# Optimization experiments

Hardware: AMD Instinct MI355X
Metric: run time of the kernel (lower is better)

Reference implementation:

```python
import jax, jax.numpy as jnp
import numpy as np

N0, N1, N2 = 200_000, 100_000, 80_000
F = 32
K5, K3 = 125, 27
M1, M2, M3, M4 = 20_000, 20_000, 30_000, 20_000
EPS = 1e-5


def sparse_conv(feats, W, in_idx, out_idx, n_out):
    """Gather-GEMM-scatter sparse conv. feats:[Nin,Cin], W:[K,Cin,Cout],
    in_idx/out_idx:[K,M] kernel map. Returns [n_out, Cout]."""
    g = feats[in_idx]                                  # [K, M, Cin] gather
    contrib = jnp.einsum('kmc,kcd->kmd', g, W)         # per-offset GEMM
    cout = W.shape[-1]
    out = jnp.zeros((n_out, cout), feats.dtype)
    return out.at[out_idx.reshape(-1)].add(contrib.reshape(-1, cout))


def bn(x, g, b):
    m = x.mean(0)
    v = x.var(0)
    return (x - m) * jax.lax.rsqrt(v + EPS) * g + b


def setup_inputs():
    key = jax.random.key(0)
    ks = jax.random.split(key, 16)
    W_SCALE = 0.02
    inp = {
        'x_feats': jax.random.normal(ks[0], (N0, 1), jnp.float32),
        'w1a': jax.random.normal(ks[1], (K5, 1, F), jnp.float32) * W_SCALE,
        'w1b': jax.random.normal(ks[2], (K5, F, F), jnp.float32) * W_SCALE,
        'w1c': jax.random.normal(ks[3], (K5, F, F), jnp.float32) * W_SCALE,
        'w2': jax.random.normal(ks[4], (K3, F, 2 * F), jnp.float32) * W_SCALE,
        'w3a': jax.random.normal(ks[5], (K3, 2 * F, 4 * F), jnp.float32) * W_SCALE,
        'w3b': jax.random.normal(ks[6], (K3, 4 * F, 8 * F), jnp.float32) * W_SCALE,
        'bn1b_g': jnp.ones((F,), jnp.float32), 'bn1b_b': jnp.zeros((F,), jnp.float32),
        'bn1c_g': jnp.ones((F,), jnp.float32), 'bn1c_b': jnp.zeros((F,), jnp.float32),
        'bn3a_g': jnp.ones((4 * F,), jnp.float32), 'bn3a_b': jnp.zeros((4 * F,), jnp.float32),
        'bn3b_g': jnp.ones((8 * F,), jnp.float32), 'bn3b_b': jnp.zeros((8 * F,), jnp.float32),
        'km1a_in': jax.random.randint(ks[7], (K5, M1), 0, N0, jnp.int32),
        'km1a_out': jax.random.randint(ks[8], (K5, M1), 0, N1, jnp.int32),
        'km1b_in': jax.random.randint(ks[9], (K5, M2), 0, N1, jnp.int32),
        'km1b_out': jax.random.randint(ks[10], (K5, M2), 0, N1, jnp.int32),
        'km1c_in': jax.random.randint(ks[11], (K5, M2), 0, N1, jnp.int32),
        'km1c_out': jax.random.randint(ks[12], (K5, M2), 0, N1, jnp.int32),
        'km2_in': jax.random.randint(ks[13], (K3, M3), 0, N1, jnp.int32),
        'km2_out': jax.random.randint(ks[14], (K3, M3), 0, N2, jnp.int32),
        'km3a_in': jax.random.randint(jax.random.fold_in(key, 20), (K3, M4), 0, N2, jnp.int32),
        'km3a_out': jax.random.randint(jax.random.fold_in(key, 21), (K3, M4), 0, N2, jnp.int32),
        'km3b_in': jax.random.randint(jax.random.fold_in(key, 22), (K3, M4), 0, N2, jnp.int32),
        'km3b_out': jax.random.randint(jax.random.fold_in(key, 23), (K3, M4), 0, N2, jnp.int32),
        'n1': N1,
        'n2': N2,
    }
    return inp


def reference(x_feats, w1a, w1b, w1c, w2, w3a, w3b,
              bn1b_g, bn1b_b, bn1c_g, bn1c_b, bn3a_g, bn3a_b, bn3b_g, bn3b_b,
              km1a_in, km1a_out, km1b_in, km1b_out, km1c_in, km1c_out,
              km2_in, km2_out, km3a_in, km3a_out, km3b_in, km3b_out, n1, n2):
    # enc1: conv(1->F, k5, s2) + ReLU
    h = jax.nn.relu(sparse_conv(x_feats, w1a, km1a_in, km1a_out, n1))
    # conv(F->F, k5) + BN + ReLU
    h = jax.nn.relu(bn(sparse_conv(h, w1b, km1b_in, km1b_out, n1), bn1b_g, bn1b_b))
    # conv(F->F, k5) + BN + ReLU
    x_e1 = jax.nn.relu(bn(sparse_conv(h, w1c, km1c_in, km1c_out, n1), bn1c_g, bn1c_b))
    # conv2: conv(F->2F, k3) onto c_out coordinates (no activation)
    h2 = sparse_conv(x_e1, w2, km2_in, km2_out, n2)
    # enc2: conv(2F->4F, k3) + BN + ReLU
    h2 = jax.nn.relu(bn(sparse_conv(h2, w3a, km3a_in, km3a_out, n2), bn3a_g, bn3a_b))
    # conv(4F->8F, k3) + BN + ReLU
    x_e2 = jax.nn.relu(bn(sparse_conv(h2, w3b, km3b_in, km3b_out, n2), bn3b_g, bn3b_b))
    return (x_e1, x_e2)
```

## Files before the change

kernel.cpp:

```cpp
#include <hip/hip_runtime.h>
#include <hip/hip_fp16.h>
#include <cstdint>
#include <algorithm>

#define N1c 100000
#define N2c 80000
#define EPSc 1e-5f
#define STRIDE_N1 102400
#define STRIDE_N2 81920

__global__ __launch_bounds__(256) void rank2d_kernel(
    const int* __restrict__ out_idx, int* __restrict__ rank,
    int* __restrict__ bins, int E, int M, int q, int stride)
{
    for (int e = blockIdx.x * 256 + threadIdx.x; e < E; e += gridDim.x * 256) {
        int chunk = (e / M) / q;
        rank[e] = atomicAdd(&bins[chunk * stride + out_idx[e]], 1);
    }
}

__global__ __launch_bounds__(256) void scan1(
    const int* __restrict__ bins, int* __restrict__ ptr,
    int* __restrict__ bsums, int n)
{
    __shared__ int lds[256];
    int base = blockIdx.x * 1024;
    int v[4]; int t = 0;
    #pragma unroll
    for (int i = 0; i < 4; ++i) {
        int idx = base + threadIdx.x * 4 + i;
        v[i] = idx < n ? bins[idx] : 0;
        t += v[i];
    }
    lds[threadIdx.x] = t; __syncthreads();
    for (int off = 1; off < 256; off <<= 1) {
        int x = threadIdx.x >= off ? lds[threadIdx.x - off] : 0;
        __syncthreads();
        lds[threadIdx.x] += x;
        __syncthreads();
    }
    int run = lds[threadIdx.x] - t;
    if (threadIdx.x == 255) bsums[blockIdx.x] = lds[255];
    #pragma unroll
    for (int i = 0; i < 4; ++i) {
        int idx = base + threadIdx.x * 4 + i;
        if (idx < n) ptr[idx] = run;
        run += v[i];
    }
}

__global__ __launch_bounds__(64) void scan2s(
    int* __restrict__ bsums, int bpc, int nch)
{
    int c = threadIdx.x;
    if (c < nch) {
        int run = 0;
        for (int i = 0; i < bpc; ++i) {
            int idx = c * bpc + i;
            int t = bsums[idx]; bsums[idx] = run; run += t;
        }
    }
}

__global__ __launch_bounds__(256) void scan3(
    int* __restrict__ ptr, const int* __restrict__ bsums, int n)
{
    int idx = blockIdx.x * 1024 + threadIdx.x * 4;
    int add = bsums[blockIdx.x];
    #pragma unroll
    for (int i = 0; i < 4; ++i)
        if (idx + i < n) ptr[idx + i] += add;
}

__global__ __launch_bounds__(256) void scatter_1a(
    const float* __restrict__ x, const int* __restrict__ iin,
    const int* __restrict__ iout, const int* __restrict__ ptr,
    const int* __restrict__ rank, float2* __restrict__ payload, int E, int M)
{
    for (int e = blockIdx.x * 256 + threadIdx.x; e < E; e += gridDim.x * 256) {
        int k = e / M;
        float2 p; p.x = x[iin[e]]; p.y = __int_as_float(k);
        payload[ptr[iout[e]] + rank[e]] = p;
    }
}

__global__ __launch_bounds__(256) void phaseB_1a(
    const float2* __restrict__ payload, const int* __restrict__ ptr,
    const float* __restrict__ W, float* __restrict__ out, int n)
{
    __shared__ float Wl[125 * 32];
    for (int i = threadIdx.x; i < 125 * 32; i += 256) Wl[i] = W[i];
    __syncthreads();
    int total = n * 32;
    for (int idx = blockIdx.x * 256 + threadIdx.x; idx < total; idx += gridDim.x * 256) {
        int o = idx >> 5, c = idx & 31;
        int s0 = ptr[o], s1 = ptr[o + 1];
        float acc = 0.f;
        for (int s = s0; s < s1; ++s) {
            float2 p = payload[s];
            acc = fmaf(p.x, Wl[(__float_as_int(p.y) << 5) + c], acc);
        }
        out[idx] = fmaxf(acc, 0.f);
    }
}

template <int CIN, int CINC, int CTILE, int WST, int TP, int TC, int GMODE>
__global__ __launch_bounds__(256) void phaseA8(
    const float* __restrict__ feats, const float* __restrict__ W,
    const int* __restrict__ in_idx, const int* __restrict__ out_idx,
    const int* __restrict__ ptr, const int* __restrict__ rank,
    __half* __restrict__ contrib, int M,
    const float* __restrict__ sc, const float* __restrict__ sh)
{
    constexpr int NCG = CTILE / TC;
    constexpr int PPG = 256 / NCG;
    constexpr int PP  = PPG * TP;
    constexpr int NCH  = CIN / CINC;
    constexpr int LOADERS = 256 / PP;
    constexpr int SITER = CINC / 4 / LOADERS;
    constexpr int FTS = PP + 4;
    static_assert(SITER >= 1, "CINC too small for loader layout");

    const int k = blockIdx.y;
    __shared__ float Wl[CINC][CTILE];
    __shared__ float ft[CINC][FTS];
    __shared__ int sslot[PP];

    const int cg = threadIdx.x % NCG;
    const int pg = threadIdx.x / NCG;
    const int p0 = pg * TP;
    const int pl = threadIdx.x % PP;
    const int ll = threadIdx.x / PP;

    const int* iin  = in_idx  + (size_t)k * M;
    const int* iout = out_idx + (size_t)k * M;
    const int* rk   = rank    + (size_t)k * M;
    const float* Wk = W + (size_t)k * CIN * WST;

    for (int base = blockIdx.x * PP; base < M; base += gridDim.x * PP) {
        float acc[TP][TC];
        #pragma unroll
        for (int p = 0; p < TP; ++p)
            #pragma unroll
            for (int c = 0; c < TC; ++c) acc[p][c] = 0.f;

        int p = base + pl;
        bool act = p < M;
        const float* fr = nullptr;
        float4 v[SITER];
        if (act) {
            fr = feats + (size_t)iin[p] * CIN;
            #pragma unroll
            for (int i = 0; i < SITER; ++i)
                v[i] = *(const float4*)(fr + (ll + i * LOADERS) * 4);
        }

        #pragma unroll
        for (int ch = 0; ch < NCH; ++ch) {
            __syncthreads();
            for (int i = threadIdx.x; i < CINC * (CTILE / 4); i += 256) {
                int j = i / (CTILE / 4), q = i % (CTILE / 4);
                int gq = q % (TC / 4);
                int cq = q / (TC / 4);
                int pq = gq * NCG + cq;
                *(float4*)&Wl[j][pq * 4] =
                    *(const float4*)(Wk + (size_t)(ch * CINC + j) * WST + q * 4);
            }
            if (act) {
                if (ch == 0 && threadIdx.x < PP)
                    sslot[pl] = ptr[iout[p]] + rk[p];
                #pragma unroll
                for (int i = 0; i < SITER; ++i) {
                    int j4 = (ll + i * LOADERS) * 4;
                    float4 w = v[i];
                    if (GMODE == 2) {
                        float4 s4 = *(const float4*)(sc + ch * CINC + j4);
                        float4 h4 = *(const float4*)(sh + ch * CINC + j4);
                        w.x = fmaxf(fmaf(w.x, s4.x, h4.x), 0.f);
                        w.y = fmaxf(fmaf(w.y, s4.y, h4.y), 0.f);
                        w.z = fmaxf(fmaf(w.z, s4.z, h4.z), 0.f);
                        w.w = fmaxf(fmaf(w.w, s4.w, h4.w), 0.f);
                    }
                    ft[j4 + 0][pl] = w.x;
                    ft[j4 + 1][pl] = w.y;
                    ft[j4 + 2][pl] = w.z;
                    ft[j4 + 3][pl] = w.w;
                }
                if (ch + 1 < NCH) {
                    #pragma unroll
                    for (int i = 0; i < SITER; ++i)
                        v[i] = *(const float4*)(fr + (ch + 1) * CINC
                                                + (ll + i * LOADERS) * 4);
                }
            }
            __syncthreads();

            #pragma unroll 4
            for (int j = 0; j < CINC; ++j) {
                float fv[TP], wv[TC];
                #pragma unroll
                for (int g = 0; g < TP / 4; ++g)
                    *(float4*)&fv[g * 4] = *(const float4*)&ft[j][p0 + g * 4];
                #pragma unroll
                for (int g = 0; g < TC / 4; ++g)
                    *(float4*)&wv[g * 4] = *(const float4*)&Wl[j][(g * NCG + cg) * 4];
                #pragma unroll
                for (int pp = 0; pp < TP; ++pp)
                    #pragma unroll
                    for (int c = 0; c < TC; ++c)
                        acc[pp][c] = fmaf(fv[pp], wv[c], acc[pp][c]);
            }
        }

        #pragma unroll
        for (int q = 0; q < TP; ++q) {
            if (base + p0 + q < M) {
                size_t s = (size_t)sslot[p0 + q];
                #pragma unroll
                for (int g = 0; g < TC / 4; ++g) {
                    __half2 h0 = __floats2half2_rn(acc[q][g * 4 + 0], acc[q][g * 4 + 1]);
                    __half2 h1 = __floats2half2_rn(acc[q][g * 4 + 2], acc[q][g * 4 + 3]);
                    uint2 pk;
                    pk.x = *(unsigned int*)&h0;
                    pk.y = *(unsigned int*)&h1;
                    *(uint2*)&contrib[s * CTILE + cg * TC + g * 4] = pk;
                }
            }
        }
    }
}

template <int CSTR, bool STATS>
__global__ __launch_bounds__(256) void phaseB8(
    const __half* __restrict__ contrib, const int* __restrict__ ptr,
    float* __restrict__ out, int n, int ostr, int accum,
    double* __restrict__ statsbuf, int sqoff)
{
    float s1 = 0.f, s2 = 0.f;
    int total = n * CSTR;
    for (int idx = blockIdx.x * 256 + threadIdx.x; idx < total; idx += gridDim.x * 256) {
        int o = idx / CSTR, c = idx % CSTR;
        int a = ptr[o], b = ptr[o + 1];
        float acc = accum ? out[(size_t)o * ostr + c] : 0.f;
        for (int s = a; s < b; ++s)
            acc += __half2float(contrib[(size_t)s * CSTR + c]);
        out[(size_t)o * ostr + c] = acc;
        if (STATS) { s1 += acc; s2 += acc * acc; }
    }
    if constexpr (STATS) {
        __shared__ double l1[256], l2[256];
        l1[threadIdx.x] = (double)s1; l2[threadIdx.x] = (double)s2;
        __syncthreads();
        for (int off = 128; off >= CSTR; off >>= 1) {
            if (threadIdx.x < (unsigned)off) {
                l1[threadIdx.x] += l1[threadIdx.x + off];
                l2[threadIdx.x] += l2[threadIdx.x + off];
            }
            __syncthreads();
        }
        if (threadIdx.x < CSTR) {
            atomicAdd(&statsbuf[threadIdx.x], l1[threadIdx.x]);
            atomicAdd(&statsbuf[sqoff + threadIdx.x], l2[threadIdx.x]);
        }
    }
}

template <int C>
__global__ __launch_bounds__(256) void make_scsh(
    const double* __restrict__ sums, const float* __restrict__ g,
    const float* __restrict__ b, float* __restrict__ sc, float* __restrict__ sh,
    double inv_n)
{
    int c = threadIdx.x;
    if (c < C) {
        double mean = sums[c] * inv_n;
        double var  = sums[C + c] * inv_n - mean * mean;
        float s = g[c] * (float)(1.0 / sqrt(var + (double)EPSc));
        sc[c] = s;
        sh[c] = b[c] - (float)mean * s;
    }
}

template <int C>
__global__ __launch_bounds__(256) void bn_apply_relu_kernel(
    float* __restrict__ x, int n, const double* __restrict__ sums,
    const float* __restrict__ g, const float* __restrict__ b)
{
    const int c = threadIdx.x % C;
    const double inv_n = 1.0 / (double)n;
    double mean = sums[c] * inv_n;
    double var  = sums[C + c] * inv_n - mean * mean;
    float scale = g[c] * (float)(1.0 / sqrt(var + (double)EPSc));
    float shift = b[c] - (float)mean * scale;
    size_t total = (size_t)n * C;
    size_t stride = (size_t)gridDim.x * 256;
    for (size_t i = (size_t)blockIdx.x * 256 + threadIdx.x; i < total; i += stride)
        x[i] = fmaxf(x[i] * scale + shift, 0.f);
}

struct Plan { int q, nch; };

static Plan make_plan(long long tot_elems, int K, long long cap, int maxch)
{
    if (cap < 1) cap = 1;
    long long nch0 = (tot_elems + cap - 1) / cap;
    if (nch0 < 1) nch0 = 1;
    if (nch0 > K) nch0 = K;
    int q = (int)((K + nch0 - 1) / nch0);
    int nch = (K + q - 1) / q;
    if (nch > maxch) { q = (K + maxch - 1) / maxch; nch = (K + q - 1) / q; }
    return { q, nch };
}

static void build_csr2d(const int* iout, int* rank, int* bins, int* ptr, int* bsums,
                        int E, int M, int q, int nch, int stride, hipStream_t s)
{
    hipMemsetAsync(bins, 0, (size_t)nch * stride * sizeof(int), s);
    int gb = std::min(2048, (E + 255) / 256);
    hipLaunchKernelGGL(rank2d_kernel, dim3(gb), dim3(256), 0, s, iout, rank, bins, E, M, q, stride);
    int totalbins = nch * stride, nb = totalbins / 1024, bpc = stride / 1024;
    hipLaunchKernelGGL(scan1, dim3(nb), dim3(256), 0, s, bins, ptr, bsums, totalbins);
    hipLaunchKernelGGL(scan2s, dim3(1), dim3(64), 0, s, bsums, bpc, nch);
    hipLaunchKernelGGL(scan3, dim3(nb), dim3(256), 0, s, ptr, bsums, totalbins);
}

template <int CIN, int CINC, int COUT, int TP, int TC, int GMODE, bool STATS>
static void run_layer(const float* feats, const float* W,
                      const int* iin, const int* iout, float* outp,
                      int M, int K, int n_out, int stride, int maxch,
                      int* bins, int* ptr, int* bsums, int* rank, __half* contrib,
                      long long cap_f32, const float* sc, const float* sh,
                      double* statsbuf, hipStream_t s)
{
    constexpr int NCG = COUT / TC;
    constexpr int PP  = (256 / NCG) * TP;
    long long cap_h = cap_f32 * 2;
    Plan pl = make_plan((long long)K * M * COUT, K, cap_h, maxch);
    build_csr2d(iout, rank, bins, ptr, bsums, K * M, M, pl.q, pl.nch, stride, s);
    for (int ch = 0; ch < pl.nch; ++ch) {
        int k0 = ch * pl.q;
        int qc = std::min(pl.q, K - k0);
        dim3 g((M + PP - 1) / PP, qc);
        hipLaunchKernelGGL((phaseA8<CIN, CINC, COUT, COUT, TP, TC, GMODE>), g, dim3(256), 0, s,
                           feats, W + (size_t)k0 * CIN * COUT,
                           iin + (size_t)k0 * M, iout + (size_t)k0 * M,
                           ptr + (size_t)ch * stride, rank + (size_t)k0 * M,
                           contrib, M, sc, sh);
        bool last = (ch == pl.nch - 1);
        if (STATS && last)
            hipLaunchKernelGGL((phaseB8<COUT, true>), dim3(2048), dim3(256), 0, s,
                               contrib, ptr + (size_t)ch * stride, outp, n_out, COUT,
                               ch ? 1 : 0, statsbuf, COUT);
        else
            hipLaunchKernelGGL((phaseB8<COUT, false>), dim3(2048), dim3(256), 0, s,
                               contrib, ptr + (size_t)ch * stride, outp, n_out, COUT,
                               ch ? 1 : 0, (double*)nullptr, 0);
    }
}

extern "C" void kernel_launch(void* const* d_in, const int* in_sizes, int n_in,
                              void* d_out, int out_size, void* d_ws, size_t ws_size,
                              hipStream_t stream)
{
    const float* x_feats = (const float*)d_in[0];
    const float* w1a = (const float*)d_in[1];
    const float* w1b = (const float*)d_in[2];
    const float* w1c = (const float*)d_in[3];
    const float* w2  = (const float*)d_in[4];
    const float* w3a = (const float*)d_in[5];
    const float* w3b = (const float*)d_in[6];
    const float* bn1b_g = (const float*)d_in[7];
    const float* bn1b_b = (const float*)d_in[8];
    const float* bn1c_g = (const float*)d_in[9];
    const float* bn1c_b = (const float*)d_in[10];
    const float* bn3a_g = (const float*)d_in[11];
    const float* bn3a_b = (const float*)d_in[12];
    const float* bn3b_g = (const float*)d_in[13];
    const float* bn3b_b = (const float*)d_in[14];
    const int* km1a_in  = (const int*)d_in[15];
    const int* km1a_out = (const int*)d_in[16];
    const int* km1b_in  = (const int*)d_in[17];
    const int* km1b_out = (const int*)d_in[18];
    const int* km1c_in  = (const int*)d_in[19];
    const int* km1c_out = (const int*)d_in[20];
    const int* km2_in   = (const int*)d_in[21];
    const int* km2_out  = (const int*)d_in[22];
    const int* km3a_in  = (const int*)d_in[23];
    const int* km3a_out = (const int*)d_in[24];
    const int* km3b_in  = (const int*)d_in[25];
    const int* km3b_out = (const int*)d_in[26];

    float* out  = (float*)d_out;
    float* x_e1 = out;
    float* x_e2 = out + (size_t)N1c * 32;

    float* ws = (float*)d_ws;
    float*  poolA  = ws;
    float*  poolB  = poolA + 10240000;
    double* dstats = (double*)(poolB + 5120000);
    float*  scsh   = (float*)(dstats + 2048);
    int*    bins   = (int*)(scsh + 1024);
    int*    ptr    = bins + 819200;
    int*    bsums  = ptr + 819200;
    int*    rank   = bsums + 1024;
    float*  contribf = (float*)(rank + 2500000);
    __half* contrib  = (__half*)contribf;
    const long long FIXED = 10240000LL + 5120000 + 4096 + 1024
                          + 819200 + 819200 + 1024 + 2500000;
    long long cap = (long long)(ws_size / 4) - FIXED - 32;
    if (cap < 1) cap = 1;

    float* h1  = poolA;
    float* h3  = poolA;
    float* h2  = poolB;
    float* h2b = poolB;

    double* dst1b = dstats;
    double* dst1c = dstats + 512;
    double* dst3a = dstats + 1024;
    double* dst3b = dstats + 1536;
    float* sc1b = scsh,       *sh1b = scsh + 32;
    float* sc3a = scsh + 256, *sh3a = scsh + 384;

    hipMemsetAsync(dstats, 0, 2048 * sizeof(double), stream);

    {
        build_csr2d(km1a_out, rank, bins, ptr, bsums, 125 * 20000, 20000, 125, 1,
                    STRIDE_N1, stream);
        hipLaunchKernelGGL(scatter_1a, dim3(2048), dim3(256), 0, stream,
                           x_feats, km1a_in, km1a_out, ptr, rank, (float2*)contribf,
                           125 * 20000, 20000);
        hipLaunchKernelGGL(phaseB_1a, dim3(2048), dim3(256), 0, stream,
                           (const float2*)contribf, ptr, w1a, h1, N1c);
    }

    run_layer<32, 32, 32, 8, 4, 0, true>(h1, w1b, km1b_in, km1b_out, h2, 20000, 125, N1c,
                                         STRIDE_N1, 8, bins, ptr, bsums, rank, contrib,
                                         cap, nullptr, nullptr, dst1b, stream);
    hipLaunchKernelGGL((make_scsh<32>), dim3(1), dim3(256), 0, stream,
                       dst1b, bn1b_g, bn1b_b, sc1b, sh1b, 1.0 / N1c);

    run_layer<32, 32, 32, 8, 4, 2, true>(h2, w1c, km1c_in, km1c_out, x_e1, 20000, 125, N1c,
                                         STRIDE_N1, 8, bins, ptr, bsums, rank, contrib,
                                         cap, sc1b, sh1b, dst1c, stream);
    hipLaunchKernelGGL((bn_apply_relu_kernel<32>), dim3(2048), dim3(256), 0, stream,
                       x_e1, N1c, dst1c, bn1c_g, bn1c_b);

    run_layer<32, 32, 64, 8, 8, 0, false>(x_e1, w2, km2_in, km2_out, h2b, 30000, 27, N2c,
                                          STRIDE_N2, 10, bins, ptr, bsums, rank, contrib,
                                          cap, nullptr, nullptr, nullptr, stream);

    run_layer<64, 32, 128, 8, 8, 0, true>(h2b, w3a, km3a_in, km3a_out, h3, 20000, 27, N2c,
                                          STRIDE_N2, 10, bins, ptr, bsums, rank, contrib,
                                          cap, nullptr, nullptr, dst3a, stream);
    hipLaunchKernelGGL((make_scsh<128>), dim3(1), dim3(256), 0, stream,
                       dst3a, bn3a_g, bn3a_b, sc3a, sh3a, 1.0 / N2c);

    {
        const int M = 20000, K = 27;
        Plan pl = make_plan((long long)K * M * 128, K, cap * 2, 10);
        build_csr2d(km3b_out, rank, bins, ptr, bsums, K * M, M, pl.q, pl.nch,
                    STRIDE_N2, stream);
        constexpr int PP = (256 / (128 / 8)) * 8;
        for (int half = 0; half < 2; ++half) {
            for (int ch = 0; ch < pl.nch; ++ch) {
                int k0 = ch * pl.q;
                int qc = std::min(pl.q, K - k0);
                dim3 g((M + PP - 1) / PP, qc);
                hipLaunchKernelGGL((phaseA8<128, 32, 128, 256, 8, 8, 2>), g, dim3(256), 0, stream,
                                   h3, w3b + half * 128 + (size_t)k0 * 128 * 256,
                                   km3b_in + (size_t)k0 * M, km3b_out + (size_t)k0 * M,
                                   ptr + (size_t)ch * STRIDE_N2, rank + (size_t)k0 * M,
                                   contrib, M, sc3a, sh3a);
                bool last = (ch == pl.nch - 1);
                if (last)
                    hipLaunchKernelGGL((phaseB8<128, true>), dim3(2048), dim3(256), 0, stream,
                                       contrib, ptr + (size_t)ch * STRIDE_N2,
                                       x_e2 + half * 128, N2c, 256, ch ? 1 : 0,
                                       dst3b + half * 128, 256);
                else
                    hipLaunchKernelGGL((phaseB8<128, false>), dim3(2048), dim3(256), 0, stream,
                                       contrib, ptr + (size_t)ch * STRIDE_N2,
                                       x_e2 + half * 128, N2c, 256, ch ? 1 : 0,
                                       (double*)nullptr, 0);
            }
        }
        hipLaunchKernelGGL((bn_apply_relu_kernel<256>), dim3(2048), dim3(256), 0, stream,
                           x_e2, N2c, dst3b, bn3b_g, bn3b_b);
    }
}
```

Measured before the change: 2.201 ms.

## Use packed fp16 dot2 for gather-GEMM inner product in phaseA8

Converts both the weight tile and the gathered feature tile to packed half2 in shared memory and replaces the fp32 FMA inner loop with v_dot2_f32_f16, which processes two input channels per instruction while accumulating in fp32. This halves LDS footprint and LDS read traffic per multiply and roughly halves ALU instruction count in the GEMM loop. It also drops the register prefetch of the next channel chunk, loading features inside each chunk instead. Inputs are rounded to fp16, which lowers precision.

Result: faster. 2.064 ms (-6.2%).

```diff
diff --git a/kernel.cpp b/kernel.cpp
--- a/kernel.cpp
+++ b/kernel.cpp
@@ -8,6 +8,18 @@
 #define EPSc 1e-5f
 #define STRIDE_N1 102400
 #define STRIDE_N2 81920
+
+typedef _Float16 half2_t __attribute__((ext_vector_type(2)));
+
+__device__ __forceinline__ float dot2(half2_t a, half2_t b, float c)
+{
+#if __has_builtin(__builtin_amdgcn_fdot2)
+    return __builtin_amdgcn_fdot2(a, b, c, false);
+#else
+    asm("v_dot2_f32_f16 %0, %1, %2, %0" : "+v"(c) : "v"(a), "v"(b));
+    return c;
+#endif
+}
 
 __global__ __launch_bounds__(256) void rank2d_kernel(
     const int* __restrict__ out_idx, int* __restrict__ rank,
@@ -120,10 +132,11 @@
     constexpr int SITER = CINC / 4 / LOADERS;
     constexpr int FTS = PP + 4;
     static_assert(SITER >= 1, "CINC too small for loader layout");
+    static_assert((CINC % 2) == 0 && (TP % 4) == 0 && (TC % 4) == 0, "");
 
     const int k = blockIdx.y;
-    __shared__ float Wl[CINC][CTILE];
-    __shared__ float ft[CINC][FTS];
+    __shared__ half2_t Wl[CINC / 2][CTILE];
+    __shared__ half2_t ft[CINC / 2][FTS];
     __shared__ int sslot[PP];
 
     const int cg = threadIdx.x % NCG;
@@ -144,71 +157,64 @@
             #pragma unroll
             for (int c = 0; c < TC; ++c) acc[p][c] = 0.f;
 
-        int p = base + pl;
-        bool act = p < M;
-        const float* fr = nullptr;
-        float4 v[SITER];
-        if (act) {
-            fr = feats + (size_t)iin[p] * CIN;
-            #pragma unroll
-            for (int i = 0; i < SITER; ++i)
-                v[i] = *(const float4*)(fr + (ll + i * LOADERS) * 4);
-        }
-
         #pragma unroll
         for (int ch = 0; ch < NCH; ++ch) {
             __syncthreads();
-            for (int i = threadIdx.x; i < CINC * (CTILE / 4); i += 256) {
-                int j = i / (CTILE / 4), q = i % (CTILE / 4);
+            for (int i = threadIdx.x; i < (CINC / 2) * (CTILE / 4); i += 256) {
+                int j2 = i / (CTILE / 4), q = i % (CTILE / 4);
                 int gq = q % (TC / 4);
                 int cq = q / (TC / 4);
                 int pq = gq * NCG + cq;
-                *(float4*)&Wl[j][pq * 4] =
-                    *(const float4*)(Wk + (size_t)(ch * CINC + j) * WST + q * 4);
-            }
-            if (act) {
+                const float* wr = Wk + (size_t)(ch * CINC + 2 * j2) * WST + q * 4;
+                float4 a = *(const float4*)wr;
+                float4 b = *(const float4*)(wr + WST);
+                half2_t t[4];
+                t[0][0] = (_Float16)a.x; t[0][1] = (_Float16)b.x;
+                t[1][0] = (_Float16)a.y; t[1][1] = (_Float16)b.y;
+                t[2][0] = (_Float16)a.z; t[2][1] = (_Float16)b.z;
+                t[3][0] = (_Float16)a.w; t[3][1] = (_Float16)b.w;
+                *(uint4*)&Wl[j2][pq * 4] = *(uint4*)t;
+            }
+            int p = base + pl;
+            if (p < M) {
                 if (ch == 0 && threadIdx.x < PP)
                     sslot[pl] = ptr[iout[p]] + rk[p];
+                const float* fr = feats + (size_t)iin[p] * CIN + ch * CINC;
                 #pragma unroll
                 for (int i = 0; i < SITER; ++i) {
                     int j4 = (ll + i * LOADERS) * 4;
-                    float4 w = v[i];
+                    float4 v = *(const float4*)(fr + j4);
                     if (GMODE == 2) {
                         float4 s4 = *(const float4*)(sc + ch * CINC + j4);
                         float4 h4 = *(const float4*)(sh + ch * CINC + j4);
-                        w.x = fmaxf(fmaf(w.x, s4.x, h4.x), 0.f);
-                        w.y = fmaxf(fmaf(w.y, s4.y, h4.y), 0.f);
-                        w.z = fmaxf(fmaf(w.z, s4.z, h4.z), 0.f);
-                        w.w = fmaxf(fmaf(w.w, s4.w, h4.w), 0.f);
+                        v.x = fmaxf(fmaf(v.x, s4.x, h4.x), 0.f);
+                        v.y = fmaxf(fmaf(v.y, s4.y, h4.y), 0.f);
+                        v.z = fmaxf(fmaf(v.z, s4.z, h4.z), 0.f);
+                        v.w = fmaxf(fmaf(v.w, s4.w, h4.w), 0.f);
                     }
-                    ft[j4 + 0][pl] = w.x;
-                    ft[j4 + 1][pl] = w.y;
-                    ft[j4 + 2][pl] = w.z;
-                    ft[j4 + 3][pl] = w.w;
+                    half2_t lo, hi;
+                    lo[0] = (_Float16)v.x; lo[1] = (_Float16)v.y;
+                    hi[0] = (_Float16)v.z; hi[1] = (_Float16)v.w;
+                    ft[j4 / 2 + 0][pl] = lo;
+                    ft[j4 / 2 + 1][pl] = hi;
                 }
-                if (ch + 1 < NCH) {
-                    #pragma unroll
-                    for (int i = 0; i < SITER; ++i)
-                        v[i] = *(const float4*)(fr + (ch + 1) * CINC
-                                                + (ll + i * LOADERS) * 4);
-                }
             }
             __syncthreads();
 
             #pragma unroll 4
-            for (int j = 0; j < CINC; ++j) {
-                float fv[TP], wv[TC];
+            for (int j2 = 0; j2 < CINC / 2; ++j2) {
+                half2_t fv[TP], wv[TC];
                 #pragma unroll
                 for (int g = 0; g < TP / 4; ++g)
-                    *(float4*)&fv[g * 4] = *(const float4*)&ft[j][p0 + g * 4];
+                    *(uint4*)&fv[g * 4] = *(const uint4*)&ft[j2][p0 + g * 4];
                 #pragma unroll
                 for (int g = 0; g < TC / 4; ++g)
-                    *(float4*)&wv[g * 4] = *(const float4*)&Wl[j][(g * NCG + cg) * 4];
+                    *(uint4*)&wv[g * 4] = *(const uint4*)&Wl[j2][(g * NCG + cg) * 4];
                 #pragma unroll
                 for (int pp = 0; pp < TP; ++pp)
                     #pragma unroll
                     for (int c = 0; c < TC; ++c)
-                        acc[pp][c] = fmaf(fv[pp], wv[c], acc[pp][c]);
+                        acc[pp][c] = dot2(fv[pp], wv[c], acc[pp][c]);
             }
         }
 
```

## Replace FP32 register-tiled gather-GEMM with fp16 MFMA kernel using swizzled LDS

Applied to the files above, without the earlier changes.

The per-offset gather-GEMM kernel (phaseA8) is rewritten to use the 16x16x32 fp16 MFMA instructions. Gathered features and weights are converted to fp16 and staged in XOR-swizzled shared memory, and each wave computes a 32-row by CTILE-column output tile. This targets the cost of scalar FP32 FMAs in the gather-GEMM stages of all layers. In exchange, inputs are rounded to fp16 before the multiply, and the contrib writes become scalar half stores instead of packed stores, which may add write traffic overhead.

Measured after the change: 1.989 ms. -9.6%, faster.

```diff
diff --git a/kernel.cpp b/kernel.cpp
--- a/kernel.cpp
+++ b/kernel.cpp
@@ -8,6 +8,9 @@
 #define EPSc 1e-5f
 #define STRIDE_N1 102400
 #define STRIDE_N2 81920
+
+typedef _Float16 fp16x8 __attribute__((ext_vector_type(8)));
+typedef float f32x4 __attribute__((ext_vector_type(4)));
 
 __global__ __launch_bounds__(256) void rank2d_kernel(
     const int* __restrict__ out_idx, int* __restrict__ rank,
@@ -104,33 +107,30 @@
     }
 }
 
-template <int CIN, int CINC, int CTILE, int WST, int TP, int TC, int GMODE>
-__global__ __launch_bounds__(256) void phaseA8(
+template <int CIN, int CTILE, int WST, int GMODE>
+__global__ __launch_bounds__(256) void phaseA_mfma(
     const float* __restrict__ feats, const float* __restrict__ W,
     const int* __restrict__ in_idx, const int* __restrict__ out_idx,
     const int* __restrict__ ptr, const int* __restrict__ rank,
     __half* __restrict__ contrib, int M,
     const float* __restrict__ sc, const float* __restrict__ sh)
 {
-    constexpr int NCG = CTILE / TC;
-    constexpr int PPG = 256 / NCG;
-    constexpr int PP  = PPG * TP;
-    constexpr int NCH  = CIN / CINC;
-    constexpr int LOADERS = 256 / PP;
-    constexpr int SITER = CINC / 4 / LOADERS;
-    constexpr int FTS = PP + 4;
-    static_assert(SITER >= 1, "CINC too small for loader layout");
-
-    const int k = blockIdx.y;
-    __shared__ float Wl[CINC][CTILE];
-    __shared__ float ft[CINC][FTS];
+    constexpr int PP  = 128;
+    constexpr int NK  = CIN / 32;
+    constexpr int NCF = CTILE / 16;
+    constexpr int NRF = 2;
+    constexpr int GCHK = (CIN * 2) / 16;
+    constexpr int GSM  = (GCHK < 8 ? GCHK : 8) - 1;
+    static_assert(CIN % 32 == 0 && CTILE % 16 == 0, "");
+
+    __shared__ __align__(16) _Float16 Gl[PP * CIN];
+    __shared__ __align__(16) _Float16 Wt[CTILE * CIN];
     __shared__ int sslot[PP];
 
-    const int cg = threadIdx.x % NCG;
-    const int pg = threadIdx.x / NCG;
-    const int p0 = pg * TP;
-    const int pl = threadIdx.x % PP;
-    const int ll = threadIdx.x / PP;
+    const int tid  = threadIdx.x;
+    const int wave = tid >> 6;
+    const int lane = tid & 63;
+    const int k    = blockIdx.y;
 
     const int* iin  = in_idx  + (size_t)k * M;
     const int* iout = out_idx + (size_t)k * M;
@@ -138,95 +138,109 @@
     const float* Wk = W + (size_t)k * CIN * WST;
 
     for (int base = blockIdx.x * PP; base < M; base += gridDim.x * PP) {
-        float acc[TP][TC];
+        if (tid < PP && base + tid < M)
+            sslot[tid] = ptr[iout[base + tid]] + rk[base + tid];
+
+        {
+            int r  = tid & (PP - 1);
+            int hh = tid >> 7;
+            int p  = base + r;
+            if (p < M) {
+                const int c0 = hh * (CIN / 2);
+                const float* fr = feats + (size_t)iin[p] * CIN + c0;
+                #pragma unroll
+                for (int c = 0; c < CIN / 2; c += 8) {
+                    float a[8];
+                    *(float4*)&a[0] = *(const float4*)(fr + c);
+                    *(float4*)&a[4] = *(const float4*)(fr + c + 4);
+                    if (GMODE == 2) {
+                        float s[8], h[8];
+                        *(float4*)&s[0] = *(const float4*)(sc + c0 + c);
+                        *(float4*)&s[4] = *(const float4*)(sc + c0 + c + 4);
+                        *(float4*)&h[0] = *(const float4*)(sh + c0 + c);
+                        *(float4*)&h[4] = *(const float4*)(sh + c0 + c + 4);
+                        #pragma unroll
+                        for (int j = 0; j < 8; ++j)
+                            a[j] = fmaxf(fmaf(a[j], s[j], h[j]), 0.f);
+                    }
+                    _Float16 t[8];
+                    #pragma unroll
+                    for (int j = 0; j < 8; ++j) t[j] = (_Float16)a[j];
+                    int col = c0 + c;
+                    int idx = r * CIN + ((((col >> 3) ^ (r & GSM))) << 3);
+                    *(uint4*)&Gl[idx] = *(uint4*)t;
+                }
+            }
+        }
+
+        for (int i = tid; i < (CTILE / 4) * (CIN / 4); i += 256) {
+            int c4 = (i % (CTILE / 4)) * 4;
+            int k4 = (i / (CTILE / 4)) * 4;
+            const float* wr = Wk + (size_t)k4 * WST + c4;
+            float a0[4], a1[4], a2[4], a3[4];
+            *(float4*)a0 = *(const float4*)wr;
+            *(float4*)a1 = *(const float4*)(wr + WST);
+            *(float4*)a2 = *(const float4*)(wr + 2 * (size_t)WST);
+            *(float4*)a3 = *(const float4*)(wr + 3 * (size_t)WST);
+            #pragma unroll
+            for (int j = 0; j < 4; ++j) {
+                _Float16 t[4] = { (_Float16)a0[j], (_Float16)a1[j],
+                                  (_Float16)a2[j], (_Float16)a3[j] };
+                int row = c4 + j;
+                int idx = row * CIN + (((k4 >> 3) ^ (row & GSM)) << 3) + (k4 & 7);
+                *(uint2*)&Wt[idx] = *(uint2*)t;
+            }
+        }
+        __syncthreads();
+
+        f32x4 acc[NRF][NCF];
         #pragma unroll
-        for (int p = 0; p < TP; ++p)
+        for (int rf = 0; rf < NRF; ++rf)
             #pragma unroll
-            for (int c = 0; c < TC; ++c) acc[p][c] = 0.f;
-
-        int p = base + pl;
-        bool act = p < M;
-        const float* fr = nullptr;
-        float4 v[SITER];
-        if (act) {
-            fr = feats + (size_t)iin[p] * CIN;
+            for (int cf = 0; cf < NCF; ++cf)
+                acc[rf][cf] = (f32x4){0.f, 0.f, 0.f, 0.f};
+
+        const int lrow = lane & 15;
+        const int lk8  = (lane >> 4) * 8;
+        const int p0   = wave * 32;
+        #pragma unroll
+        for (int kk = 0; kk < NK; ++kk) {
+            int col = kk * 32 + lk8;
+            fp16x8 afr[NRF];
             #pragma unroll
-            for (int i = 0; i < SITER; ++i)
-                v[i] = *(const float4*)(fr + (ll + i * LOADERS) * 4);
+            for (int rf = 0; rf < NRF; ++rf) {
+                int r = p0 + rf * 16 + lrow;
+                afr[rf] = *(const fp16x8*)
+                    &Gl[r * CIN + (((col >> 3) ^ (r & GSM)) << 3)];
+            }
+            #pragma unroll
+            for (int cf = 0; cf < NCF; ++cf) {
+                int r = cf * 16 + lrow;
+                fp16x8 bfr = *(const fp16x8*)
+                    &Wt[r * CIN + (((col >> 3) ^ (r & GSM)) << 3)];
+                #pragma unroll
+                for (int rf = 0; rf < NRF; ++rf)
+                    acc[rf][cf] = __builtin_amdgcn_mfma_f32_16x16x32_f16(
+                        afr[rf], bfr, acc[rf][cf], 0, 0, 0);
+            }
         }
 
         #pragma unroll
-        for (int ch = 0; ch < NCH; ++ch) {
-            __syncthreads();
-            for (int i = threadIdx.x; i < CINC * (CTILE / 4); i += 256) {
-                int j = i / (CTILE / 4), q = i % (CTILE / 4);
-                int gq = q % (TC / 4);
-                int cq = q / (TC / 4);
-                int pq = gq * NCG + cq;
-                *(float4*)&Wl[j][pq * 4] =
-                    *(const float4*)(Wk + (size_t)(ch * CINC + j) * WST + q * 4);
-            }
-            if (act) {
-                if (ch == 0 && threadIdx.x < PP)
-                    sslot[pl] = ptr[iout[p]] + rk[p];
-                #pragma unroll
-                for (int i = 0; i < SITER; ++i) {
-                    int j4 = (ll + i * LOADERS) * 4;
-                    float4 w = v[i];
-                    if (GMODE == 2) {
-                        float4 s4 = *(const float4*)(sc + ch * CINC + j4);
-                        float4 h4 = *(const float4*)(sh + ch * CINC + j4);
-                        w.x = fmaxf(fmaf(w.x, s4.x, h4.x), 0.f);
-                        w.y = fmaxf(fmaf(w.y, s4.y, h4.y), 0.f);
-                        w.z = fmaxf(fmaf(w.z, s4.z, h4.z), 0.f);
-                        w.w = fmaxf(fmaf(w.w, s4.w, h4.w), 0.f);
-                    }
-                    ft[j4 + 0][pl] = w.x;
-                    ft[j4 + 1][pl] = w.y;
-                    ft[j4 + 2][pl] = w.z;
-                    ft[j4 + 3][pl] = w.w;
+        for (int rf = 0; rf < NRF; ++rf) {
+            int prb = p0 + rf * 16 + (lane >> 4) * 4;
+            #pragma unroll
+            for (int b = 0; b < 4; ++b) {
+                int pr = prb + b;
+                if (base + pr < M) {
+                    size_t s = (size_t)sslot[pr];
+                    #pragma unroll
+                    for (int cf = 0; cf < NCF; ++cf)
+                        contrib[s * CTILE + cf * 16 + lrow] =
+                            __float2half(acc[rf][cf][b]);
                 }
-                if (ch + 1 < NCH) {
-                    #pragma unroll
-                    for (int i = 0; i < SITER; ++i)
-                        v[i] = *(const float4*)(fr + (ch + 1) * CINC
-                                                + (ll + i * LOADERS) * 4);
-                }
-            }
-            __syncthreads();
-
-            #pragma unroll 4
-            for (int j = 0; j < CINC; ++j) {
-                float fv[TP], wv[TC];
-                #pragma unroll
-                for (int g = 0; g < TP / 4; ++g)
-                    *(float4*)&fv[g * 4] = *(const float4*)&ft[j][p0 + g * 4];
-                #pragma unroll
-                for (int g = 0; g < TC / 4; ++g)
-                    *(float4*)&wv[g * 4] = *(const float4*)&Wl[j][(g * NCG + cg) * 4];
-                #pragma unroll
-                for (int pp = 0; pp < TP; ++pp)
-                    #pragma unroll
-                    for (int c = 0; c < TC; ++c)
-                        acc[pp][c] = fmaf(fv[pp], wv[c], acc[pp][c]);
-            }
-        }
-
-        #pragma unroll
-        for (int q = 0; q < TP; ++q) {
-            if (base + p0 + q < M) {
-                size_t s = (size_t)sslot[p0 + q];
-                #pragma unroll
-                for (int g = 0; g < TC / 4; ++g) {
-                    __half2 h0 = __floats2half2_rn(acc[q][g * 4 + 0], acc[q][g * 4 + 1]);
-                    __half2 h1 = __floats2half2_rn(acc[q][g * 4 + 2], acc[q][g * 4 + 3]);
-                    uint2 pk;
-                    pk.x = *(unsigned int*)&h0;
-                    pk.y = *(unsigned int*)&h1;
-                    *(uint2*)&contrib[s * CTILE + cg * TC + g * 4] = pk;
-                }
-            }
-        }
+            }
+        }
+        __syncthreads();
     }
 }
 
@@ -324,7 +338,7 @@
     hipLaunchKernelGGL(scan3, dim3(nb), dim3(256), 0, s, ptr, bsums, totalbins);
 }
 
-template <int CIN, int CINC, int COUT, int TP, int TC, int GMODE, bool STATS>
+template <int CIN, int COUT, int GMODE, bool STATS>
 static void run_layer(const float* feats, const float* W,
                       const int* iin, const int* iout, float* outp,
                       int M, int K, int n_out, int stride, int maxch,
@@ -332,16 +346,14 @@
                       long long cap_f32, const float* sc, const float* sh,
                       double* statsbuf, hipStream_t s)
 {
-    constexpr int NCG = COUT / TC;
-    constexpr int PP  = (256 / NCG) * TP;
     long long cap_h = cap_f32 * 2;
     Plan pl = make_plan((long long)K * M * COUT, K, cap_h, maxch);
     build_csr2d(iout, rank, bins, ptr, bsums, K * M, M, pl.q, pl.nch, stride, s);
     for (int ch = 0; ch < pl.nch; ++ch) {
         int k0 = ch * pl.q;
         int qc = std::min(pl.q, K - k0);
-        dim3 g((M + PP - 1) / PP, qc);
-        hipLaunchKernelGGL((phaseA8<CIN, CINC, COUT, COUT, TP, TC, GMODE>), g, dim3(256), 0, s,
+        dim3 g((M + 127) / 128, qc);
+        hipLaunchKernelGGL((phaseA_mfma<CIN, COUT, COUT, GMODE>), g, dim3(256), 0, s,
                            feats, W + (size_t)k0 * CIN * COUT,
                            iin + (size_t)k0 * M, iout + (size_t)k0 * M,
                            ptr + (size_t)ch * stride, rank + (size_t)k0 * M,
@@ -434,25 +446,25 @@
                            (const float2*)contribf, ptr, w1a, h1, N1c);
     }
 
-    run_layer<32, 32, 32, 8, 4, 0, true>(h1, w1b, km1b_in, km1b_out, h2, 20000, 125, N1c,
-                                         STRIDE_N1, 8, bins, ptr, bsums, rank, contrib,
-                                         cap, nullptr, nullptr, dst1b, stream);
+    run_layer<32, 32, 0, true>(h1, w1b, km1b_in, km1b_out, h2, 20000, 125, N1c,
+                               STRIDE_N1, 8, bins, ptr, bsums, rank, contrib,
+                               cap, nullptr, nullptr, dst1b, stream);
     hipLaunchKernelGGL((make_scsh<32>), dim3(1), dim3(256), 0, stream,
                        dst1b, bn1b_g, bn1b_b, sc1b, sh1b, 1.0 / N1c);
 
-    run_layer<32, 32, 32, 8, 4, 2, true>(h2, w1c, km1c_in, km1c_out, x_e1, 20000, 125, N1c,
-                                         STRIDE_N1, 8, bins, ptr, bsums, rank, contrib,
-                                         cap, sc1b, sh1b, dst1c, stream);
+    run_layer<32, 32, 2, true>(h2, w1c, km1c_in, km1c_out, x_e1, 20000, 125, N1c,
+                               STRIDE_N1, 8, bins, ptr, bsums, rank, contrib,
+                               cap, sc1b, sh1b, dst1c, stream);
     hipLaunchKernelGGL((bn_apply_relu_kernel<32>), dim3(2048), dim3(256), 0, stream,
                        x_e1, N1c, dst1c, bn1c_g, bn1c_b);
 
-    run_layer<32, 32, 64, 8, 8, 0, false>(x_e1, w2, km2_in, km2_out, h2b, 30000, 27, N2c,
-                                          STRIDE_N2, 10, bins, ptr, bsums, rank, contrib,
-                                          cap, nullptr, nullptr, nullptr, stream);
-
-    run_layer<64, 32, 128, 8, 8, 0, true>(h2b, w3a, km3a_in, km3a_out, h3, 20000, 27, N2c,
-                                          STRIDE_N2, 10, bins, ptr, bsums, rank, contrib,
-                                          cap, nullptr, nullptr, dst3a, stream);
+    run_layer<32, 64, 0, false>(x_e1, w2, km2_in, km2_out, h2b, 30000, 27, N2c,
+                                STRIDE_N2, 10, bins, ptr, bsums, rank, contrib,
+                                cap, nullptr, nullptr, nullptr, stream);
+
+    run_layer<64, 128, 0, true>(h2b, w3a, km3a_in, km3a_out, h3, 20000, 27, N2c,
+                                STRIDE_N2, 10, bins, ptr, bsums, rank, contrib,
+                                cap, nullptr, nullptr, dst3a, stream);
     hipLaunchKernelGGL((make_scsh<128>), dim3(1), dim3(256), 0, stream,
                        dst3a, bn3a_g, bn3a_b, sc3a, sh3a, 1.0 / N2c);
 
@@ -461,13 +473,12 @@
         Plan pl = make_plan((long long)K * M * 128, K, cap * 2, 10);
         build_csr2d(km3b_out, rank, bins, ptr, bsums, K * M, M, pl.q, pl.nch,
                     STRIDE_N2, stream);
-        constexpr int PP = (256 / (128 / 8)) * 8;
         for (int half = 0; half < 2; ++half) {
             for (int ch = 0; ch < pl.nch; ++ch) {
                 int k0 = ch * pl.q;
                 int qc = std::min(pl.q, K - k0);
-                dim3 g((M + PP - 1) / PP, qc);
-                hipLaunchKernelGGL((phaseA8<128, 32, 128, 256, 8, 8, 2>), g, dim3(256), 0, stream,
+                dim3 g((20000 + 127) / 128, qc);
+                hipLaunchKernelGGL((phaseA_mfma<128, 128, 256, 2>), g, dim3(256), 0, stream,
                                    h3, w3b + half * 128 + (size_t)k0 * 128 * 256,
                                    km3b_in + (size_t)k0 * M, km3b_out + (size_t)k0 * M,
                                    ptr + (size_t)ch * STRIDE_N2, rank + (size_t)k0 * M,
```
